# Kernel tuning notes

Measured on AMD Instinct MI355X. Metric: run time of the kernel, lower is better.

## Reference

```python
import jax, jax.numpy as jnp
import numpy as np

H = 16          # num heads
HD = 64         # head dim
TEMPERATURE = 1.0
LN_EPS = 1e-5

def setup_inputs() -> dict:
    key = jax.random.key(0)
    ks = jax.random.split(key, 5)
    B, S, D = 2, 2048, 1024
    s = 1.0 / np.sqrt(D)
    return {
        "x": jax.random.normal(ks[0], (B, S, D), jnp.float32),
        "Wq": jax.random.normal(ks[1], (D, D), jnp.float32) * s,
        "bq": jnp.zeros((D,), jnp.float32),
        "Wk": jax.random.normal(ks[2], (D, D), jnp.float32) * s,
        "bk": jnp.zeros((D,), jnp.float32),
        "Wv": jax.random.normal(ks[3], (D, D), jnp.float32) * s,
        "bv": jnp.zeros((D,), jnp.float32),
        "Wo": jax.random.normal(ks[4], (D, D), jnp.float32) * s,
        "bo": jnp.zeros((D,), jnp.float32),
        "ln_gamma": jnp.ones((D,), jnp.float32),
        "ln_beta": jnp.zeros((D,), jnp.float32),
    }

def reference(x, Wq, bq, Wk, bk, Wv, bv, Wo, bo, ln_gamma, ln_beta):
    B, S, D = x.shape
    # LayerNorm (pre-attention)
    mu = jnp.mean(x, axis=-1, keepdims=True)
    var = jnp.mean(jnp.square(x - mu), axis=-1, keepdims=True)
    xn = (x - mu) * jax.lax.rsqrt(var + LN_EPS) * ln_gamma + ln_beta
    # Fused QKV projections (equivalent to H per-head Linears concatenated)
    q = (xn @ Wq + bq).reshape(B, S, H, HD)
    k = (xn @ Wk + bk).reshape(B, S, H, HD)
    v = (xn @ Wv + bv).reshape(B, S, H, HD)
    scale = np.sqrt(HD) * TEMPERATURE
    scores = jnp.einsum("bqhd,bkhd->bhqk", q, k) / scale
    attn = jax.nn.softmax(scores, axis=-1)  # dropout p=0 -> identity
    ctx = jnp.einsum("bhqk,bkhd->bqhd", attn, v).reshape(B, S, D)
    out = ctx @ Wo + bo
    return x + out
```

## Files before the change

kernel.cpp:

```cpp
#include <hip/hip_runtime.h>
#include <hip/hip_bf16.h>

#define Bc   2
#define Sc   2048
#define Dc   1024
#define Hc   16
#define HDc  64
#define MR   (Bc * Sc)
#define TBK  32
#define LOG2E 1.44269504088896f

typedef __attribute__((ext_vector_type(8))) short bf16x8;
typedef __attribute__((ext_vector_type(4))) float f32x4;
typedef __attribute__((ext_vector_type(4))) unsigned int u32x4;

__device__ __forceinline__ unsigned short f2bf(float f) {
    __hip_bfloat16 h = __float2bfloat16(f);
    return *reinterpret_cast<unsigned short*>(&h);
}

__device__ __forceinline__ void gll16(const unsigned short* g, unsigned short* l) {
    __builtin_amdgcn_global_load_lds(
        (__attribute__((address_space(1))) const unsigned int*)g,
        (__attribute__((address_space(3))) unsigned int*)l,
        16, 0, 0);
}

__global__ __launch_bounds__(256) void prep_kernel(
        const float* __restrict__ x, const float* __restrict__ gamma,
        const float* __restrict__ beta, unsigned short* __restrict__ xn,
        const float* __restrict__ W0, const float* __restrict__ W1,
        const float* __restrict__ W2, const float* __restrict__ W3,
        unsigned short* __restrict__ T0, unsigned short* __restrict__ T1,
        unsigned short* __restrict__ T2, unsigned short* __restrict__ T3) {
    __shared__ float tile[64][65];
    int idx = blockIdx.x;
    int t = threadIdx.x;

    if (idx < 1024) {
        int z = idx >> 8, rem = idx & 255;
        const float* W = (z == 0) ? W0 : (z == 1) ? W1 : (z == 2) ? W2 : W3;
        unsigned short* T = (z == 0) ? T0 : (z == 1) ? T1 : (z == 2) ? T2 : T3;
        int nb = (rem & 15) * 64, kb = (rem >> 4) * 64;
        int r0 = t >> 4, c4 = (t & 15) * 4;
        #pragma unroll
        for (int rr = 0; rr < 4; rr++) {
            int row = rr * 16 + r0;
            float4 v = *(const float4*)(W + (size_t)(kb + row) * Dc + nb + c4);
            tile[row][c4 + 0] = v.x; tile[row][c4 + 1] = v.y;
            tile[row][c4 + 2] = v.z; tile[row][c4 + 3] = v.w;
        }
        __syncthreads();
        #pragma unroll
        for (int rr = 0; rr < 4; rr++) {
            int nrow = rr * 16 + r0;
            ushort4 o;
            o.x = f2bf(tile[c4 + 0][nrow]); o.y = f2bf(tile[c4 + 1][nrow]);
            o.z = f2bf(tile[c4 + 2][nrow]); o.w = f2bf(tile[c4 + 3][nrow]);
            *(ushort4*)(T + (size_t)(nb + nrow) * Dc + kb + c4) = o;
        }
    } else {
        int row = idx - 1024;
        const float4* xr = (const float4*)(x + (size_t)row * Dc);
        float4 v = xr[t];
        float s  = v.x + v.y + v.z + v.w;
        float ss = v.x * v.x + v.y * v.y + v.z * v.z + v.w * v.w;
        #pragma unroll
        for (int off = 32; off; off >>= 1) {
            s  += __shfl_xor(s, off, 64);
            ss += __shfl_xor(ss, off, 64);
        }
        float* red = tile[0];
        int w = t >> 6, lane = t & 63;
        if (lane == 0) { red[w * 2] = s; red[w * 2 + 1] = ss; }
        __syncthreads();
        s  = red[0] + red[2] + red[4] + red[6];
        ss = red[1] + red[3] + red[5] + red[7];
        float mean = s * (1.0f / Dc);
        float var  = ss * (1.0f / Dc) - mean * mean;
        float rstd = rsqrtf(var + 1e-5f);
        float4 g = ((const float4*)gamma)[t], bb = ((const float4*)beta)[t];
        ushort4 o;
        o.x = f2bf((v.x - mean) * rstd * g.x + bb.x);
        o.y = f2bf((v.y - mean) * rstd * g.y + bb.y);
        o.z = f2bf((v.z - mean) * rstd * g.z + bb.z);
        o.w = f2bf((v.w - mean) * rstd * g.w + bb.w);
        *(ushort4*)(xn + (size_t)row * Dc + t * 4) = o;
    }
}

__device__ __forceinline__ void gemm_core(const unsigned short* __restrict__ A,
                                          const unsigned short* __restrict__ Wt,
                                          unsigned short* As, unsigned short* Bs,
                                          int m0, int n0, f32x4 acc[4][4]) {
    int t = threadIdx.x;
    int w = t >> 6, lane = t & 63;
    int l16 = lane & 15, quad = lane >> 4;
    int wm = (w >> 1) * 64, wn = (w & 1) * 64;

    int srow = lane >> 2;
    int scol = (lane & 3) * 8;
    const unsigned short* Ag = A  + (size_t)(m0 + w * 16 + srow) * Dc + scol;
    const unsigned short* Bg = Wt + (size_t)(n0 + w * 16 + srow) * Dc + scol;
    unsigned short* Asw = As + (w * 16) * TBK;
    unsigned short* Bsw = Bs + (w * 16) * TBK;

    for (int k0 = 0; k0 < Dc; k0 += TBK) {
        gll16(Ag + k0, Asw);
        gll16(Ag + k0 + (size_t)64 * Dc, Asw + 64 * TBK);
        gll16(Bg + k0, Bsw);
        gll16(Bg + k0 + (size_t)64 * Dc, Bsw + 64 * TBK);
        __syncthreads();
        bf16x8 af[4], bfr[4];
        #pragma unroll
        for (int i = 0; i < 4; i++) {
            af[i]  = *(const bf16x8*)(As + (wm + i * 16 + l16) * TBK + quad * 8);
            bfr[i] = *(const bf16x8*)(Bs + (wn + i * 16 + l16) * TBK + quad * 8);
        }
        #pragma unroll
        for (int i = 0; i < 4; i++)
            #pragma unroll
            for (int j = 0; j < 4; j++)
                acc[i][j] = __builtin_amdgcn_mfma_f32_16x16x32_bf16(af[i], bfr[j], acc[i][j], 0, 0, 0);
        __syncthreads();
    }
}

__global__ __launch_bounds__(256) void gemm_qkv_kernel(
        const unsigned short* __restrict__ A,
        const unsigned short* __restrict__ Wqt, const unsigned short* __restrict__ Wkt,
        const unsigned short* __restrict__ Wvt,
        const float* __restrict__ bq, const float* __restrict__ bk,
        const float* __restrict__ bv,
        unsigned short* __restrict__ Qb, unsigned short* __restrict__ Kb,
        unsigned short* __restrict__ Vtb) {
    __shared__ unsigned short As[128 * TBK];
    __shared__ unsigned short Bs[128 * TBK];
    int z = blockIdx.z;
    const unsigned short* Wt = (z == 0) ? Wqt : (z == 1) ? Wkt : Wvt;
    const float* bias = (z == 0) ? bq : (z == 1) ? bk : bv;
    unsigned short* Out = (z == 0) ? Qb : (z == 1) ? Kb : Vtb;
    float outscale = (z == 0) ? (0.125f * LOG2E) : 1.0f;

    int n0 = blockIdx.x * 128, m0 = blockIdx.y * 128;
    f32x4 acc[4][4];
    #pragma unroll
    for (int i = 0; i < 4; i++)
        #pragma unroll
        for (int j = 0; j < 4; j++) acc[i][j] = (f32x4){0.f, 0.f, 0.f, 0.f};

    gemm_core(A, Wt, As, Bs, m0, n0, acc);

    int t = threadIdx.x;
    int w = t >> 6, lane = t & 63;
    int l16 = lane & 15, quad = lane >> 4;
    int wm = (w >> 1) * 64, wn = (w & 1) * 64;
    int b = m0 >> 11;
    #pragma unroll
    for (int j = 0; j < 4; j++) {
        int col = n0 + wn + j * 16 + l16;
        float bb = bias[col];
        int h = col >> 6, d = col & 63;
        #pragma unroll
        for (int i = 0; i < 4; i++) {
            #pragma unroll
            for (int r = 0; r < 4; r++) {
                int row = m0 + wm + i * 16 + quad * 4 + r;
                int s = row & (Sc - 1);
                unsigned short v = f2bf((acc[i][j][r] + bb) * outscale);
                if (z != 2)
                    Out[(((size_t)(b * Hc + h)) * Sc + s) * HDc + d] = v;
                else
                    Out[(((size_t)(b * Hc + h)) * HDc + d) * Sc + s] = v;
            }
        }
    }
}

__global__ __launch_bounds__(256) void gemm_o_kernel(
        const unsigned short* __restrict__ A,
        const unsigned short* __restrict__ Wot,
        const float* __restrict__ bo, const float* __restrict__ resid,
        float* __restrict__ Out) {
    __shared__ unsigned short As[64 * TBK];
    __shared__ unsigned short Bs[128 * TBK];
    int t = threadIdx.x;
    int w = t >> 6, lane = t & 63;
    int l16 = lane & 15, quad = lane >> 4;
    int wm = (w >> 1) * 32, wn = (w & 1) * 64;
    int n0 = blockIdx.x * 128, m0 = blockIdx.y * 64;

    f32x4 acc[2][4];
    #pragma unroll
    for (int i = 0; i < 2; i++)
        #pragma unroll
        for (int j = 0; j < 4; j++) acc[i][j] = (f32x4){0.f, 0.f, 0.f, 0.f};

    int srow = lane >> 2;
    int scol = (lane & 3) * 8;
    const unsigned short* Ag = A   + (size_t)(m0 + w * 16 + srow) * Dc + scol;
    const unsigned short* Bg = Wot + (size_t)(n0 + w * 16 + srow) * Dc + scol;
    unsigned short* Asw = As + (w * 16) * TBK;
    unsigned short* Bsw = Bs + (w * 16) * TBK;

    for (int k0 = 0; k0 < Dc; k0 += TBK) {
        gll16(Ag + k0, Asw);
        gll16(Bg + k0, Bsw);
        gll16(Bg + k0 + (size_t)64 * Dc, Bsw + 64 * TBK);
        __syncthreads();
        bf16x8 af[2], bfr[4];
        #pragma unroll
        for (int i = 0; i < 2; i++)
            af[i]  = *(const bf16x8*)(As + (wm + i * 16 + l16) * TBK + quad * 8);
        #pragma unroll
        for (int j = 0; j < 4; j++)
            bfr[j] = *(const bf16x8*)(Bs + (wn + j * 16 + l16) * TBK + quad * 8);
        #pragma unroll
        for (int i = 0; i < 2; i++)
            #pragma unroll
            for (int j = 0; j < 4; j++)
                acc[i][j] = __builtin_amdgcn_mfma_f32_16x16x32_bf16(af[i], bfr[j], acc[i][j], 0, 0, 0);
        __syncthreads();
    }

    #pragma unroll
    for (int j = 0; j < 4; j++) {
        int col = n0 + wn + j * 16 + l16;
        float bb = bo[col];
        #pragma unroll
        for (int i = 0; i < 2; i++) {
            #pragma unroll
            for (int r = 0; r < 4; r++) {
                int row = m0 + wm + i * 16 + quad * 4 + r;
                size_t off = (size_t)row * Dc + col;
                Out[off] = acc[i][j][r] + bb + resid[off];
            }
        }
    }
}

#define BKa 64

__global__ __launch_bounds__(256, 2) void attn_mfma_kernel(
        const unsigned short* __restrict__ Q,
        const unsigned short* __restrict__ K,
        const unsigned short* __restrict__ Vt,
        unsigned short* __restrict__ O) {
    __shared__ unsigned short Ks[BKa * 64];
    __shared__ unsigned short Vs[HDc * 64];

    int t = threadIdx.x;
    int w = t >> 6, lane = t & 63;
    int quad = lane >> 4, l16 = lane & 15;

    int bid = blockIdx.x + gridDim.x * blockIdx.y;
    int q0 = (bid >> 5) * 128;
    int bh = bid & 31;
    size_t qkbase = (size_t)bh * Sc * HDc;
    size_t vbase  = (size_t)bh * HDc * Sc;

    bf16x8 qf[2][2];
    #pragma unroll
    for (int jq = 0; jq < 2; jq++) {
        const unsigned short* qr = Q + qkbase
            + (size_t)(q0 + w * 32 + jq * 16 + l16) * HDc + quad * 8;
        qf[jq][0] = *(const bf16x8*)(qr);
        qf[jq][1] = *(const bf16x8*)(qr + 32);
    }

    f32x4 Oacc[2][4];
    #pragma unroll
    for (int jq = 0; jq < 2; jq++)
        #pragma unroll
        for (int n = 0; n < 4; n++) Oacc[jq][n] = (f32x4){0.f, 0.f, 0.f, 0.f};
    float lacc[2] = {0.f, 0.f};

    int srow = t >> 2, sseg = t & 3;
    const unsigned short* Kg = K + qkbase + (size_t)srow * HDc + sseg * 16;
    const unsigned short* Vg = Vt + vbase + (size_t)srow * Sc + sseg * 16;
    int rk = srow & 7;
    unsigned short* ksw0 = Ks + srow * 64 + ((2 * sseg)     ^ rk) * 8;
    unsigned short* ksw1 = Ks + srow * 64 + ((2 * sseg + 1) ^ rk) * 8;
    unsigned short* vsw0 = Vs + srow * 64 + ((2 * sseg)     ^ rk) * 8;
    unsigned short* vsw1 = Vs + srow * 64 + ((2 * sseg + 1) ^ rk) * 8;
    int rm = l16 & 7;
    const int NT = Sc / BKa;

    bf16x8 kv0 = *(const bf16x8*)(Kg);
    bf16x8 kv1 = *(const bf16x8*)(Kg + 8);
    bf16x8 vv0 = *(const bf16x8*)(Vg);
    bf16x8 vv1 = *(const bf16x8*)(Vg + 8);

    for (int kt = 0; kt < NT; kt++) {
        __syncthreads();
        *(bf16x8*)(ksw0) = kv0;
        *(bf16x8*)(ksw1) = kv1;
        *(bf16x8*)(vsw0) = vv0;
        *(bf16x8*)(vsw1) = vv1;
        __syncthreads();

        int ktn = (kt + 1 < NT) ? kt + 1 : kt;
        const unsigned short* kgn = Kg + (size_t)ktn * BKa * HDc;
        const unsigned short* vgn = Vg + ktn * BKa;
        kv0 = *(const bf16x8*)(kgn);
        kv1 = *(const bf16x8*)(kgn + 8);
        vv0 = *(const bf16x8*)(vgn);
        vv1 = *(const bf16x8*)(vgn + 8);

        f32x4 st[2][4];
        __builtin_amdgcn_s_setprio(1);
        #pragma unroll
        for (int m = 0; m < 4; m++) {
            const unsigned short* kr = Ks + (m * 16 + l16) * 64;
            bf16x8 kf0 = *(const bf16x8*)(kr + ((quad)     ^ rm) * 8);
            bf16x8 kf1 = *(const bf16x8*)(kr + ((quad + 4) ^ rm) * 8);
            #pragma unroll
            for (int jq = 0; jq < 2; jq++) {
                f32x4 s = (f32x4){0.f, 0.f, 0.f, 0.f};
                s = __builtin_amdgcn_mfma_f32_16x16x32_bf16(kf0, qf[jq][0], s, 0, 0, 0);
                s = __builtin_amdgcn_mfma_f32_16x16x32_bf16(kf1, qf[jq][1], s, 0, 0, 0);
                st[jq][m] = s;
            }
        }
        __builtin_amdgcn_s_setprio(0);

        u32x4 pa[2][2];
        #pragma unroll
        for (int jq = 0; jq < 2; jq++) {
            float e[4][4];
            #pragma unroll
            for (int m = 0; m < 4; m++) {
                e[m][0] = __builtin_amdgcn_exp2f(st[jq][m][0]);
                e[m][1] = __builtin_amdgcn_exp2f(st[jq][m][1]);
                e[m][2] = __builtin_amdgcn_exp2f(st[jq][m][2]);
                e[m][3] = __builtin_amdgcn_exp2f(st[jq][m][3]);
                lacc[jq] += (e[m][0] + e[m][1]) + (e[m][2] + e[m][3]);
            }
            #pragma unroll
            for (int kk = 0; kk < 2; kk++) {
                unsigned int A, B, C, D;
                asm("v_cvt_pk_bf16_f32 %0, %1, %2"
                    : "=v"(A) : "v"(e[2 * kk][0]), "v"(e[2 * kk][1]));
                asm("v_cvt_pk_bf16_f32 %0, %1, %2"
                    : "=v"(B) : "v"(e[2 * kk][2]), "v"(e[2 * kk][3]));
                asm("v_cvt_pk_bf16_f32 %0, %1, %2"
                    : "=v"(C) : "v"(e[2 * kk + 1][0]), "v"(e[2 * kk + 1][1]));
                asm("v_cvt_pk_bf16_f32 %0, %1, %2"
                    : "=v"(D) : "v"(e[2 * kk + 1][2]), "v"(e[2 * kk + 1][3]));
                asm("v_permlane32_swap_b32 %0, %1" : "+v"(A), "+v"(C));
                asm("v_permlane32_swap_b32 %0, %1" : "+v"(B), "+v"(D));
                asm("v_permlane16_swap_b32 %0, %1" : "+v"(A), "+v"(C));
                asm("v_permlane16_swap_b32 %0, %1" : "+v"(B), "+v"(D));
                pa[jq][kk] = (u32x4){A, B, C, D};
            }
        }

        __builtin_amdgcn_s_setprio(1);
        #pragma unroll
        for (int kk = 0; kk < 2; kk++) {
            bf16x8 vf[4];
            #pragma unroll
            for (int n = 0; n < 4; n++)
                vf[n] = *(const bf16x8*)(Vs + (n * 16 + l16) * 64
                                         + ((4 * kk + quad) ^ rm) * 8);
            #pragma unroll
            for (int jq = 0; jq < 2; jq++) {
                bf16x8 pf = *reinterpret_cast<const bf16x8*>(&pa[jq][kk]);
                #pragma unroll
                for (int n = 0; n < 4; n++)
                    Oacc[jq][n] = __builtin_amdgcn_mfma_f32_16x16x32_bf16(pf, vf[n], Oacc[jq][n], 0, 0, 0);
            }
        }
        __builtin_amdgcn_s_setprio(0);
    }

    int b = bh >> 4, h = bh & 15;
    #pragma unroll
    for (int jq = 0; jq < 2; jq++) {
        lacc[jq] += __shfl_xor(lacc[jq], 16, 64);
        lacc[jq] += __shfl_xor(lacc[jq], 32, 64);
        #pragma unroll
        for (int i = 0; i < 4; i++) {
            float li = __shfl(lacc[jq], quad * 4 + i, 64);
            float rl = 1.0f / li;
            int q = q0 + w * 32 + jq * 16 + quad * 4 + i;
            #pragma unroll
            for (int n = 0; n < 4; n++) {
                O[((size_t)(b * Sc + q)) * Dc + h * HDc + n * 16 + l16] =
                    f2bf(Oacc[jq][n][i] * rl);
            }
        }
    }
}

extern "C" void kernel_launch(void* const* d_in, const int* in_sizes, int n_in,
                              void* d_out, int out_size, void* d_ws, size_t ws_size,
                              hipStream_t stream) {
    const float* x     = (const float*)d_in[0];
    const float* Wq    = (const float*)d_in[1];
    const float* bq    = (const float*)d_in[2];
    const float* Wk    = (const float*)d_in[3];
    const float* bk    = (const float*)d_in[4];
    const float* Wv    = (const float*)d_in[5];
    const float* bv    = (const float*)d_in[6];
    const float* Wo    = (const float*)d_in[7];
    const float* bo    = (const float*)d_in[8];
    const float* gamma = (const float*)d_in[9];
    const float* beta  = (const float*)d_in[10];
    float* out = (float*)d_out;

    unsigned short* us = (unsigned short*)d_ws;
    const size_t NE = (size_t)MR * Dc;
    const size_t WE = (size_t)Dc * Dc;
    unsigned short* xn  = us;
    unsigned short* Qb  = us + NE;
    unsigned short* Kb  = us + 2 * NE;
    unsigned short* Vtb = us + 3 * NE;
    unsigned short* ctx = us + 4 * NE;
    unsigned short* Wqt = us + 5 * NE;
    unsigned short* Wkt = Wqt + WE;
    unsigned short* Wvt = Wkt + WE;
    unsigned short* Wot = Wvt + WE;

    prep_kernel<<<1024 + MR, 256, 0, stream>>>(x, gamma, beta, xn,
                                               Wq, Wk, Wv, Wo,
                                               Wqt, Wkt, Wvt, Wot);

    dim3 qkvgrid(Dc / 128, MR / 128, 3);
    gemm_qkv_kernel<<<qkvgrid, 256, 0, stream>>>(xn, Wqt, Wkt, Wvt, bq, bk, bv,
                                                 Qb, Kb, Vtb);

    dim3 agrid(Sc / 128, Bc * Hc);
    attn_mfma_kernel<<<agrid, 256, 0, stream>>>(Qb, Kb, Vtb, ctx);

    dim3 ogrid(Dc / 128, MR / 64);
    gemm_o_kernel<<<ogrid, 256, 0, stream>>>(ctx, Wot, bo, x, out);
}
```

Before: 199.3 us.

## Rewrite QKV GEMM with 256x256 tiles, double-buffered LDS and XOR swizzle

```diff
diff --git a/kernel.cpp b/kernel.cpp
--- a/kernel.cpp
+++ b/kernel.cpp
@@ -89,44 +89,23 @@
     }
 }
 
-__device__ __forceinline__ void gemm_core(const unsigned short* __restrict__ A,
-                                          const unsigned short* __restrict__ Wt,
-                                          unsigned short* As, unsigned short* Bs,
-                                          int m0, int n0, f32x4 acc[4][4]) {
-    int t = threadIdx.x;
-    int w = t >> 6, lane = t & 63;
-    int l16 = lane & 15, quad = lane >> 4;
-    int wm = (w >> 1) * 64, wn = (w & 1) * 64;
-
-    int srow = lane >> 2;
-    int scol = (lane & 3) * 8;
-    const unsigned short* Ag = A  + (size_t)(m0 + w * 16 + srow) * Dc + scol;
-    const unsigned short* Bg = Wt + (size_t)(n0 + w * 16 + srow) * Dc + scol;
-    unsigned short* Asw = As + (w * 16) * TBK;
-    unsigned short* Bsw = Bs + (w * 16) * TBK;
-
-    for (int k0 = 0; k0 < Dc; k0 += TBK) {
-        gll16(Ag + k0, Asw);
-        gll16(Ag + k0 + (size_t)64 * Dc, Asw + 64 * TBK);
-        gll16(Bg + k0, Bsw);
-        gll16(Bg + k0 + (size_t)64 * Dc, Bsw + 64 * TBK);
-        __syncthreads();
-        bf16x8 af[4], bfr[4];
-        #pragma unroll
-        for (int i = 0; i < 4; i++) {
-            af[i]  = *(const bf16x8*)(As + (wm + i * 16 + l16) * TBK + quad * 8);
-            bfr[i] = *(const bf16x8*)(Bs + (wn + i * 16 + l16) * TBK + quad * 8);
-        }
-        #pragma unroll
-        for (int i = 0; i < 4; i++)
-            #pragma unroll
-            for (int j = 0; j < 4; j++)
-                acc[i][j] = __builtin_amdgcn_mfma_f32_16x16x32_bf16(af[i], bfr[j], acc[i][j], 0, 0, 0);
-        __syncthreads();
-    }
-}
-
-__global__ __launch_bounds__(256) void gemm_qkv_kernel(
+#define QBM 256
+#define QBN 256
+#define QBK 64
+
+__device__ __forceinline__ void qstage(const unsigned short* Ab,
+                                       const unsigned short* Bb,
+                                       unsigned short* la, unsigned short* lb,
+                                       int tw, int ko) {
+    #pragma unroll
+    for (int c = 0; c < 4; c++)
+        gll16(Ab + (size_t)c * 64 * Dc + ko, la + (c * 64 + tw * 8) * QBK);
+    #pragma unroll
+    for (int c = 0; c < 4; c++)
+        gll16(Bb + (size_t)c * 64 * Dc + ko, lb + (c * 64 + tw * 8) * QBK);
+}
+
+__global__ __launch_bounds__(512, 2) void gemm_qkv_kernel(
         const unsigned short* __restrict__ A,
         const unsigned short* __restrict__ Wqt, const unsigned short* __restrict__ Wkt,
         const unsigned short* __restrict__ Wvt,
@@ -134,27 +113,76 @@
         const float* __restrict__ bv,
         unsigned short* __restrict__ Qb, unsigned short* __restrict__ Kb,
         unsigned short* __restrict__ Vtb) {
-    __shared__ unsigned short As[128 * TBK];
-    __shared__ unsigned short Bs[128 * TBK];
+    __shared__ unsigned short LA[2][QBM * QBK];
+    __shared__ unsigned short LB[2][QBN * QBK];
     int z = blockIdx.z;
     const unsigned short* Wt = (z == 0) ? Wqt : (z == 1) ? Wkt : Wvt;
     const float* bias = (z == 0) ? bq : (z == 1) ? bk : bv;
     unsigned short* Out = (z == 0) ? Qb : (z == 1) ? Kb : Vtb;
     float outscale = (z == 0) ? (0.125f * LOG2E) : 1.0f;
 
-    int n0 = blockIdx.x * 128, m0 = blockIdx.y * 128;
-    f32x4 acc[4][4];
-    #pragma unroll
-    for (int i = 0; i < 4; i++)
+    int n0 = blockIdx.x * QBN, m0 = blockIdx.y * QBM;
+    int t = threadIdx.x;
+    int tw = t >> 6, ln = t & 63;
+    int quad = ln >> 4, l16 = ln & 15;
+    int wm = (tw >> 2) * 128, wn = (tw & 3) * 64;
+
+    int lr = ln >> 3;
+    int ls = (ln & 7) ^ lr;
+    const unsigned short* Ab = A  + (size_t)(m0 + tw * 8 + lr) * Dc + ls * 8;
+    const unsigned short* Bb = Wt + (size_t)(n0 + tw * 8 + lr) * Dc + ls * 8;
+
+    f32x4 acc[8][4];
+    #pragma unroll
+    for (int i = 0; i < 8; i++)
         #pragma unroll
         for (int j = 0; j < 4; j++) acc[i][j] = (f32x4){0.f, 0.f, 0.f, 0.f};
 
-    gemm_core(A, Wt, As, Bs, m0, n0, acc);
-
-    int t = threadIdx.x;
-    int w = t >> 6, lane = t & 63;
-    int l16 = lane & 15, quad = lane >> 4;
-    int wm = (w >> 1) * 64, wn = (w & 1) * 64;
+    const int NKT = Dc / QBK;
+
+    qstage(Ab, Bb, LA[0], LB[0], tw, 0);
+    qstage(Ab, Bb, LA[1], LB[1], tw, QBK);
+
+    int rm8 = l16 & 7;
+    for (int kt = 0; kt < NKT; kt++) {
+        int buf = kt & 1;
+        const unsigned short* LAb = LA[buf];
+        const unsigned short* LBb = LB[buf];
+        if (kt == NKT - 1) asm volatile("s_waitcnt vmcnt(0)" ::: "memory");
+        else               asm volatile("s_waitcnt vmcnt(8)" ::: "memory");
+        __builtin_amdgcn_sched_barrier(0);
+        __builtin_amdgcn_s_barrier();
+        __builtin_amdgcn_sched_barrier(0);
+
+        #pragma unroll
+        for (int kk = 0; kk < 2; kk++) {
+            #pragma unroll
+            for (int h = 0; h < 2; h++) {
+                int sl = ((kk * 4 + quad) ^ rm8) * 8;
+                bf16x8 a[4], b[4];
+                #pragma unroll
+                for (int i = 0; i < 4; i++)
+                    a[i] = *(const bf16x8*)&LAb[(wm + (h * 4 + i) * 16 + l16) * QBK + sl];
+                #pragma unroll
+                for (int j = 0; j < 4; j++)
+                    b[j] = *(const bf16x8*)&LBb[(wn + j * 16 + l16) * QBK + sl];
+                __builtin_amdgcn_s_setprio(1);
+                #pragma unroll
+                for (int i = 0; i < 4; i++)
+                    #pragma unroll
+                    for (int j = 0; j < 4; j++)
+                        acc[h * 4 + i][j] = __builtin_amdgcn_mfma_f32_16x16x32_bf16(
+                            a[i], b[j], acc[h * 4 + i][j], 0, 0, 0);
+                __builtin_amdgcn_s_setprio(0);
+                __builtin_amdgcn_sched_barrier(0);
+            }
+        }
+        __builtin_amdgcn_s_barrier();
+        __builtin_amdgcn_sched_barrier(0);
+        if (kt + 2 < NKT)
+            qstage(Ab, Bb, LA[buf], LB[buf], tw, (kt + 2) * QBK);
+    }
+
     int b = m0 >> 11;
     #pragma unroll
     for (int j = 0; j < 4; j++) {
@@ -162,7 +190,7 @@
         float bb = bias[col];
         int h = col >> 6, d = col & 63;
         #pragma unroll
-        for (int i = 0; i < 4; i++) {
+        for (int i = 0; i < 8; i++) {
             #pragma unroll
             for (int r = 0; r < 4; r++) {
                 int row = m0 + wm + i * 16 + quad * 4 + r;
@@ -426,8 +454,8 @@
                                                Wq, Wk, Wv, Wo,
                                                Wqt, Wkt, Wvt, Wot);
 
-    dim3 qkvgrid(Dc / 128, MR / 128, 3);
-    gemm_qkv_kernel<<<qkvgrid, 256, 0, stream>>>(xn, Wqt, Wkt, Wvt, bq, bk, bv,
+    dim3 qkvgrid(Dc / QBN, MR / QBM, 3);
+    gemm_qkv_kernel<<<qkvgrid, 512, 0, stream>>>(xn, Wqt, Wkt, Wvt, bq, bk, bv,
                                                  Qb, Kb, Vtb);
 
     dim3 agrid(Sc / 128, Bc * Hc);
```

Result: slower. 217.7 us (+9.2%).
